# Performance work log

Hardware: AMD Instinct MI355X
Metric: run time of the kernel (lower is better)

## Reference

```python
import jax, jax.numpy as jnp
import numpy as np

N_NODES = 50000
N_EDGES = 1600000
D = 128


def setup_inputs() -> dict:
    key = jax.random.key(0)
    ks = jax.random.split(key, 12)
    feats = jax.random.normal(ks[0], (N_NODES, D), dtype=jnp.float32)
    src = jax.random.randint(ks[1], (N_EDGES,), 0, N_NODES)
    dst = jax.random.randint(ks[2], (N_EDGES,), 0, N_NODES)
    s = 1.0 / np.sqrt(D)
    inp = {"feats": feats, "src": src, "dst": dst}
    for i, k0 in enumerate(range(3, 12, 3)):
        inp[f"w_self{i}"] = jax.random.normal(ks[k0], (D, D), dtype=jnp.float32) * s
        inp[f"w_neigh{i}"] = jax.random.normal(ks[k0 + 1], (D, D), dtype=jnp.float32) * s
        inp[f"b{i}"] = jnp.zeros((D,), dtype=jnp.float32)
    return inp


def _sage_layer(h, src, dst, deg, w_self, w_neigh, b, act):
    # mean aggregation over incoming edges: gather src feats, scatter-sum to dst
    neigh_sum = jax.ops.segment_sum(h[src], dst, num_segments=N_NODES)  # [N, d]
    neigh = neigh_sum / deg[:, None]  # zero-degree nodes stay 0 (deg clamped to 1)
    out = h @ w_self + neigh @ w_neigh + b
    return jax.nn.relu(out) if act else out


def reference(feats, src, dst, w_self0, w_neigh0, b0, w_self1, w_neigh1, b1, w_self2, w_neigh2, b2):
    ones = jnp.ones((src.shape[0],), dtype=feats.dtype)
    deg = jax.ops.segment_sum(ones, dst, num_segments=N_NODES)
    deg = jnp.maximum(deg, 1.0)
    h = _sage_layer(feats, src, dst, deg, w_self0, w_neigh0, b0, True)
    h = _sage_layer(h, src, dst, deg, w_self1, w_neigh1, b1, True)
    h = _sage_layer(h, src, dst, deg, w_self2, w_neigh2, b2, False)
    return h
```

## Files before the change

### kernel.cpp

```cpp
#include <hip/hip_runtime.h>
#include <hip/hip_bf16.h>

#define N_NODES 50000
#define N_EDGES 1600000
#define DF 128
#define EPB 2500
#define B1 640
#define NBIN 196

typedef __attribute__((ext_vector_type(8))) short short8v;
typedef __attribute__((ext_vector_type(4))) float float4v;

__device__ __forceinline__ ushort bf16rne(float f) {
    uint u = __float_as_uint(f);
    return (ushort)((u + 0x7fffu + ((u >> 16) & 1u)) >> 16);
}


__global__ __launch_bounds__(256) void h1_kernel(const int* __restrict__ dst,
                                                 int* __restrict__ gh) {
    __shared__ int hist[NBIN];
    const int tid = threadIdx.x;
    const int blk = blockIdx.x;
    if (tid < NBIN) hist[tid] = 0;
    __syncthreads();
    const int lo = blk * EPB, hiE = min(lo + EPB, N_EDGES);
    for (int i = lo + tid; i < hiE; i += 256) atomicAdd(&hist[dst[i] >> 8], 1);
    __syncthreads();
    if (tid < NBIN) gh[tid * B1 + blk] = hist[tid];
}

__global__ __launch_bounds__(256) void scanA_kernel(int* __restrict__ gh,
                                                    int* __restrict__ rowtot) {
    __shared__ int buf[256];
    __shared__ int carry_s;
    const int tid = threadIdx.x;
    const int d = blockIdx.x;
    if (tid == 0) carry_s = 0;
    __syncthreads();
    for (int base = 0; base < B1; base += 256) {
        int idx = base + tid;
        int v = (idx < B1) ? gh[d * B1 + idx] : 0;
        buf[tid] = v;
        __syncthreads();
#pragma unroll
        for (int off = 1; off < 256; off <<= 1) {
            int t = (tid >= off) ? buf[tid - off] : 0;
            __syncthreads();
            buf[tid] += t;
            __syncthreads();
        }
        int carry = carry_s;
        if (idx < B1) gh[d * B1 + idx] = carry + buf[tid] - v;
        int tot = buf[255];
        __syncthreads();
        if (tid == 0) carry_s = carry + tot;
        __syncthreads();
    }
    if (tid == 0) rowtot[d] = carry_s;
}

__global__ __launch_bounds__(256) void scanB_kernel(const int* __restrict__ rowtot,
                                                    int* __restrict__ rowbase) {
    __shared__ int buf[256];
    const int tid = threadIdx.x;
    int v = (tid < NBIN) ? rowtot[tid] : 0;
    buf[tid] = v;
    __syncthreads();
#pragma unroll
    for (int off = 1; off < 256; off <<= 1) {
        int t = (tid >= off) ? buf[tid - off] : 0;
        __syncthreads();
        buf[tid] += t;
        __syncthreads();
    }
    if (tid < NBIN) rowbase[tid] = buf[tid] - v;
    if (tid == 0) rowbase[NBIN] = buf[255];
}

__global__ __launch_bounds__(256) void scatter1_kernel(const int* __restrict__ src,
                                                       const int* __restrict__ dst,
                                                       const int* __restrict__ gh,
                                                       const int* __restrict__ rowbase,
                                                       uint2* __restrict__ tmp) {
    __shared__ int cur[NBIN];
    const int tid = threadIdx.x;
    const int blk = blockIdx.x;
    if (tid < NBIN) cur[tid] = rowbase[tid] + gh[tid * B1 + blk];
    __syncthreads();
    const int lo = blk * EPB, hiE = min(lo + EPB, N_EDGES);
    for (int i = lo + tid; i < hiE; i += 256) {
        int d = dst[i];
        int pos = atomicAdd(&cur[d >> 8], 1);
        uint2 v;
        v.x = (uint)src[i];
        v.y = (uint)d;
        tmp[pos] = v;
    }
}

__global__ __launch_bounds__(256) void pass2_kernel(const uint2* __restrict__ tmp,
                                                    const int* __restrict__ rowbase,
                                                    int* __restrict__ deg,
                                                    int* __restrict__ rstart,
                                                    int* __restrict__ adj,
                                                    int* __restrict__ counter) {
    __shared__ int hist[256];
    __shared__ int sbuf[256];
    __shared__ int cur2[256];
    __shared__ int base_s;
    const int tid = threadIdx.x;
    const int hi = blockIdx.x;
    const int s = rowbase[hi], e = rowbase[hi + 1];
    hist[tid] = 0;
    __syncthreads();
    for (int i = s + tid; i < e; i += 256) atomicAdd(&hist[tmp[i].y & 255u], 1);
    __syncthreads();
    int h = hist[tid];
    int v = (h + 3) & ~3;
    sbuf[tid] = v;
    __syncthreads();
#pragma unroll
    for (int off = 1; off < 256; off <<= 1) {
        int t = (tid >= off) ? sbuf[tid - off] : 0;
        __syncthreads();
        sbuf[tid] += t;
        __syncthreads();
    }
    if (tid == 255) base_s = atomicAdd(counter, sbuf[255]);
    __syncthreads();
    int rs = base_s + sbuf[tid] - v;
    int n = hi * 256 + tid;
    if (n < N_NODES) {
        deg[n] = h;
        rstart[n] = rs;
    }
    cur2[tid] = rs;
    __syncthreads();
    for (int i = s + tid; i < e; i += 256) {
        uint2 t2 = tmp[i];
        int pos = atomicAdd(&cur2[t2.y & 255u], 1);
        adj[pos] = (int)t2.x;
    }
}


__global__ __launch_bounds__(256) void conv_kernel(const float* __restrict__ h,
                                                   ushort* __restrict__ hb) {
    int i = blockIdx.x * 256 + threadIdx.x;
    const int total = N_NODES * DF / 4;
    if (i < total) {
        float4 v = ((const float4*)h)[i];
        ushort4 o;
        o.x = bf16rne(v.x); o.y = bf16rne(v.y);
        o.z = bf16rne(v.z); o.w = bf16rne(v.w);
        ((ushort4*)hb)[i] = o;
    }
}


__global__ __launch_bounds__(256) void wprep_kernel(const float* __restrict__ wS,
                                                    const float* __restrict__ wN,
                                                    ushort* __restrict__ Wt) {
    int idx = blockIdx.x * 256 + threadIdx.x;
    if (idx < 128 * 256) {
        int c = idx >> 8;
        int k = idx & 255;
        float v = (k < 128) ? wS[k * 128 + c] : wN[(k - 128) * 128 + c];
        Wt[c * 256 + k] = bf16rne(v);
    }
}


__global__ __launch_bounds__(256) void agg_kernel(const ushort* __restrict__ hb,
                                                  const int* __restrict__ rstart,
                                                  const int* __restrict__ degv,
                                                  const int* __restrict__ adj,
                                                  ushort* __restrict__ neighb) {
    const int wave = threadIdx.x >> 6;
    const int lane = threadIdx.x & 63;
    const int n = blockIdx.x * 4 + wave;
    if (n >= N_NODES) return;
    const int s = rstart[n];
    const int d = degv[n];
    const int q = lane >> 4;
    const int f = lane & 15;
    const size_t foff = (size_t)(f * 8);

    float acc[8];
#pragma unroll
    for (int j = 0; j < 8; j++) acc[j] = 0.f;

#define GATHER_ADD(EIDX)                                                    \
    {                                                                       \
        int e_ = adj[(EIDX)];                                               \
        uint4 u_ = *(const uint4*)&hb[(size_t)e_ * DF + foff];              \
        acc[0] += __uint_as_float(u_.x << 16);                              \
        acc[1] += __uint_as_float(u_.x & 0xffff0000u);                      \
        acc[2] += __uint_as_float(u_.y << 16);                              \
        acc[3] += __uint_as_float(u_.y & 0xffff0000u);                      \
        acc[4] += __uint_as_float(u_.z << 16);                              \
        acc[5] += __uint_as_float(u_.z & 0xffff0000u);                      \
        acc[6] += __uint_as_float(u_.w << 16);                              \
        acc[7] += __uint_as_float(u_.w & 0xffff0000u);                      \
    }

    int i = 0;
    for (; i + 16 <= d; i += 16) {
        GATHER_ADD(s + i + q)
        GATHER_ADD(s + i + 4 + q)
        GATHER_ADD(s + i + 8 + q)
        GATHER_ADD(s + i + 12 + q)
    }
    for (; i + 4 <= d; i += 4) {
        GATHER_ADD(s + i + q)
    }
    if (i < d) {
        int r = d - i;
        if (q < r) GATHER_ADD(s + i + q)
    }
#undef GATHER_ADD

#pragma unroll
    for (int j = 0; j < 8; j++) {
        acc[j] += __shfl_xor(acc[j], 16, 64);
        acc[j] += __shfl_xor(acc[j], 32, 64);
    }

    if (q == 0) {
        float inv = 1.0f / (float)(d < 1 ? 1 : d);
        uint4 o;
        o.x = (uint)bf16rne(acc[0] * inv) | ((uint)bf16rne(acc[1] * inv) << 16);
        o.y = (uint)bf16rne(acc[2] * inv) | ((uint)bf16rne(acc[3] * inv) << 16);
        o.z = (uint)bf16rne(acc[4] * inv) | ((uint)bf16rne(acc[5] * inv) << 16);
        o.w = (uint)bf16rne(acc[6] * inv) | ((uint)bf16rne(acc[7] * inv) << 16);
        *(uint4*)&neighb[(size_t)n * DF + foff] = o;
    }
}


template <bool RELU, bool FP32OUT>
__global__ __launch_bounds__(256, 2) void gemm_mfma(const ushort* __restrict__ hbin,
                                                    const ushort* __restrict__ neighb,
                                                    const ushort* __restrict__ Wt,
                                                    const float* __restrict__ bias,
                                                    float* __restrict__ out32,
                                                    ushort* __restrict__ outbf) {
    __shared__ ushort As[64 * 40];
    __shared__ ushort Bs[128 * 40];
    const int tid = threadIdx.x;
    const int lane = tid & 63;
    const int w = tid >> 6;
    const int nbase = blockIdx.x * 64;
    const int l15 = lane & 15, l4 = lane >> 4;

    float4v acc[4][2];
#pragma unroll
    for (int i = 0; i < 4; i++)
#pragma unroll
        for (int j = 0; j < 2; j++) acc[i][j] = (float4v)0.f;

    for (int ks = 0; ks < 8; ++ks) {
        const int k0 = ks * 32;
        const ushort* Xsrc = (ks < 4) ? hbin : neighb;
        const int kk = k0 & 127;
        if (ks) __syncthreads();
        {
            int r = tid >> 2, cp = tid & 3;
            int gn = nbase + r;
            if (gn > N_NODES - 1) gn = N_NODES - 1;
            *(uint4*)&As[r * 40 + cp * 8] =
                *(const uint4*)&Xsrc[(size_t)gn * 128 + kk + cp * 8];
        }
#pragma unroll
        for (int j = 0; j < 2; j++) {
            int ch = tid + j * 256;
            int r = ch >> 2, cp = ch & 3;
            *(uint4*)&Bs[r * 40 + cp * 8] =
                *(const uint4*)&Wt[(size_t)r * 256 + k0 + cp * 8];
        }
        __syncthreads();
        short8v a[4], b[2];
#pragma unroll
        for (int i = 0; i < 4; i++)
            a[i] = *(const short8v*)&As[(i * 16 + l15) * 40 + l4 * 8];
#pragma unroll
        for (int j = 0; j < 2; j++)
            b[j] = *(const short8v*)&Bs[(w * 32 + j * 16 + l15) * 40 + l4 * 8];
#pragma unroll
        for (int i = 0; i < 4; i++)
#pragma unroll
            for (int j = 0; j < 2; j++)
                acc[i][j] = __builtin_amdgcn_mfma_f32_16x16x32_bf16(
                    a[i], b[j], acc[i][j], 0, 0, 0);
    }

#pragma unroll
    for (int j = 0; j < 2; j++) {
        int col = w * 32 + j * 16 + l15;
        float bv = bias[col];
#pragma unroll
        for (int i = 0; i < 4; i++) {
            int row0 = nbase + i * 16 + l4 * 4;
#pragma unroll
            for (int r = 0; r < 4; r++) {
                int row = row0 + r;
                if (row < N_NODES) {
                    float v = acc[i][j][r] + bv;
                    if (RELU) v = fmaxf(v, 0.f);
                    if (FP32OUT) {
                        out32[(size_t)row * 128 + col] = v;
                    } else {
                        outbf[(size_t)row * 128 + col] = bf16rne(v);
                    }
                }
            }
        }
    }
}


extern "C" void kernel_launch(void* const* d_in, const int* in_sizes, int n_in,
                              void* d_out, int out_size, void* d_ws, size_t ws_size,
                              hipStream_t stream) {
    const float* feats = (const float*)d_in[0];
    const int* src = (const int*)d_in[1];
    const int* dst = (const int*)d_in[2];
    const float* wS[3] = {(const float*)d_in[3], (const float*)d_in[6], (const float*)d_in[9]};
    const float* wN[3] = {(const float*)d_in[4], (const float*)d_in[7], (const float*)d_in[10]};
    const float* bb[3] = {(const float*)d_in[5], (const float*)d_in[8], (const float*)d_in[11]};
    float* out = (float*)d_out;

    char* p = (char*)d_ws;
    auto alloc = [&](size_t bytes) {
        char* r = p;
        p += (bytes + 255) & ~(size_t)255;
        return r;
    };
    ushort* hbA = (ushort*)alloc((size_t)N_NODES * DF * sizeof(ushort));
    ushort* hbB = (ushort*)alloc((size_t)N_NODES * DF * sizeof(ushort));
    ushort* neighb = (ushort*)alloc((size_t)N_NODES * DF * sizeof(ushort));
    ushort* Wt = (ushort*)alloc((size_t)3 * 128 * 256 * sizeof(ushort));
    uint2* tmp = (uint2*)alloc((size_t)N_EDGES * sizeof(uint2));
    int* gh = (int*)alloc((size_t)NBIN * B1 * sizeof(int));
    int* rowtot = (int*)alloc((size_t)NBIN * sizeof(int));
    int* rowbase = (int*)alloc((size_t)(NBIN + 1) * sizeof(int));
    int* deg = (int*)alloc((size_t)N_NODES * sizeof(int));
    int* rstart = (int*)alloc((size_t)N_NODES * sizeof(int));
    int* counter = (int*)alloc(sizeof(int));
    int* adj = (int*)alloc((size_t)(N_EDGES + 4 * N_NODES) * sizeof(int));

    const int CB = (N_NODES * DF / 4 + 255) / 256;
    const int WB = (128 * 256 + 255) / 256;

    hipMemsetAsync(counter, 0, sizeof(int), stream);
    h1_kernel<<<B1, 256, 0, stream>>>(dst, gh);
    scanA_kernel<<<NBIN, 256, 0, stream>>>(gh, rowtot);
    scanB_kernel<<<1, 256, 0, stream>>>(rowtot, rowbase);
    scatter1_kernel<<<B1, 256, 0, stream>>>(src, dst, gh, rowbase, tmp);
    pass2_kernel<<<NBIN, 256, 0, stream>>>(tmp, rowbase, deg, rstart, adj, counter);

    wprep_kernel<<<WB, 256, 0, stream>>>(wS[0], wN[0], Wt);
    wprep_kernel<<<WB, 256, 0, stream>>>(wS[1], wN[1], Wt + 128 * 256);
    wprep_kernel<<<WB, 256, 0, stream>>>(wS[2], wN[2], Wt + 2 * 128 * 256);
    conv_kernel<<<CB, 256, 0, stream>>>(feats, hbA);

    const int AGG_GRID = (N_NODES + 3) / 4;
    const int GB = (N_NODES + 63) / 64;

    agg_kernel<<<AGG_GRID, 256, 0, stream>>>(hbA, rstart, deg, adj, neighb);
    gemm_mfma<true, false><<<GB, 256, 0, stream>>>(hbA, neighb, Wt, bb[0], nullptr, hbB);
    agg_kernel<<<AGG_GRID, 256, 0, stream>>>(hbB, rstart, deg, adj, neighb);
    gemm_mfma<true, false><<<GB, 256, 0, stream>>>(hbB, neighb, Wt + 128 * 256, bb[1], nullptr, hbA);
    agg_kernel<<<AGG_GRID, 256, 0, stream>>>(hbA, rstart, deg, adj, neighb);
    gemm_mfma<false, true><<<GB, 256, 0, stream>>>(hbA, neighb, Wt + 2 * 128 * 256, bb[2], out, nullptr);
}
```

Baseline: 345.6 us.

## Fuse neighbor aggregation into GEMM layer kernel and merge prep kernels

Each layer's mean-aggregation is moved into the MFMA GEMM kernel. Each block gathers neighbor sums for its 64 rows into shared memory and uses them directly as the second half of the K dimension, which removes the neighb global round-trip and one launch per layer. The weight-transpose and feature-conversion kernels are merged into a single prep kernel, and the counter memset is folded into scanB. The trade-off is lower parallelism in the gather: 782 blocks each loop over 16 nodes per wave, instead of 12500 blocks with one node per wave. The larger shared-memory footprint may also cut occupancy and latency hiding for the random gathers.

```diff
diff --git a/kernel.cpp b/kernel.cpp
--- a/kernel.cpp
+++ b/kernel.cpp
@@ -61,7 +61,8 @@
 }
 
 __global__ __launch_bounds__(256) void scanB_kernel(const int* __restrict__ rowtot,
-                                                    int* __restrict__ rowbase) {
+                                                    int* __restrict__ rowbase,
+                                                    int* __restrict__ counter) {
     __shared__ int buf[256];
     const int tid = threadIdx.x;
     int v = (tid < NBIN) ? rowtot[tid] : 0;
@@ -75,7 +76,10 @@
         __syncthreads();
     }
     if (tid < NBIN) rowbase[tid] = buf[tid] - v;
-    if (tid == 0) rowbase[NBIN] = buf[255];
+    if (tid == 0) {
+        rowbase[NBIN] = buf[255];
+        counter[0] = 0;
+    }
 }
 
 __global__ __launch_bounds__(256) void scatter1_kernel(const int* __restrict__ src,
@@ -145,132 +149,133 @@
 }
 
 
-__global__ __launch_bounds__(256) void conv_kernel(const float* __restrict__ h,
-                                                   ushort* __restrict__ hb) {
-    int i = blockIdx.x * 256 + threadIdx.x;
-    const int total = N_NODES * DF / 4;
-    if (i < total) {
-        float4 v = ((const float4*)h)[i];
+#define CONV_TOT (N_NODES * DF / 4)
+#define WPREP_TOT (3 * 128 * 256)
+
+__global__ __launch_bounds__(256) void prep_kernel(const float* __restrict__ feats,
+                                                   ushort* __restrict__ hb,
+                                                   const float* __restrict__ wS0,
+                                                   const float* __restrict__ wN0,
+                                                   const float* __restrict__ wS1,
+                                                   const float* __restrict__ wN1,
+                                                   const float* __restrict__ wS2,
+                                                   const float* __restrict__ wN2,
+                                                   ushort* __restrict__ Wt) {
+    int gid = blockIdx.x * 256 + threadIdx.x;
+    if (gid < CONV_TOT) {
+        float4 v = ((const float4*)feats)[gid];
         ushort4 o;
         o.x = bf16rne(v.x); o.y = bf16rne(v.y);
         o.z = bf16rne(v.z); o.w = bf16rne(v.w);
-        ((ushort4*)hb)[i] = o;
-    }
-}
-
-
-__global__ __launch_bounds__(256) void wprep_kernel(const float* __restrict__ wS,
-                                                    const float* __restrict__ wN,
-                                                    ushort* __restrict__ Wt) {
-    int idx = blockIdx.x * 256 + threadIdx.x;
-    if (idx < 128 * 256) {
-        int c = idx >> 8;
-        int k = idx & 255;
-        float v = (k < 128) ? wS[k * 128 + c] : wN[(k - 128) * 128 + c];
-        Wt[c * 256 + k] = bf16rne(v);
-    }
-}
-
-
-__global__ __launch_bounds__(256) void agg_kernel(const ushort* __restrict__ hb,
-                                                  const int* __restrict__ rstart,
-                                                  const int* __restrict__ degv,
-                                                  const int* __restrict__ adj,
-                                                  ushort* __restrict__ neighb) {
-    const int wave = threadIdx.x >> 6;
-    const int lane = threadIdx.x & 63;
-    const int n = blockIdx.x * 4 + wave;
-    if (n >= N_NODES) return;
-    const int s = rstart[n];
-    const int d = degv[n];
-    const int q = lane >> 4;
-    const int f = lane & 15;
-    const size_t foff = (size_t)(f * 8);
-
-    float acc[8];
-#pragma unroll
-    for (int j = 0; j < 8; j++) acc[j] = 0.f;
-
-#define GATHER_ADD(EIDX)                                                    \
-    {                                                                       \
-        int e_ = adj[(EIDX)];                                               \
-        uint4 u_ = *(const uint4*)&hb[(size_t)e_ * DF + foff];              \
-        acc[0] += __uint_as_float(u_.x << 16);                              \
-        acc[1] += __uint_as_float(u_.x & 0xffff0000u);                      \
-        acc[2] += __uint_as_float(u_.y << 16);                              \
-        acc[3] += __uint_as_float(u_.y & 0xffff0000u);                      \
-        acc[4] += __uint_as_float(u_.z << 16);                              \
-        acc[5] += __uint_as_float(u_.z & 0xffff0000u);                      \
-        acc[6] += __uint_as_float(u_.w << 16);                              \
-        acc[7] += __uint_as_float(u_.w & 0xffff0000u);                      \
-    }
-
-    int i = 0;
-    for (; i + 16 <= d; i += 16) {
-        GATHER_ADD(s + i + q)
-        GATHER_ADD(s + i + 4 + q)
-        GATHER_ADD(s + i + 8 + q)
-        GATHER_ADD(s + i + 12 + q)
-    }
-    for (; i + 4 <= d; i += 4) {
-        GATHER_ADD(s + i + q)
-    }
-    if (i < d) {
-        int r = d - i;
-        if (q < r) GATHER_ADD(s + i + q)
-    }
-#undef GATHER_ADD
-
-#pragma unroll
-    for (int j = 0; j < 8; j++) {
-        acc[j] += __shfl_xor(acc[j], 16, 64);
-        acc[j] += __shfl_xor(acc[j], 32, 64);
-    }
-
-    if (q == 0) {
-        float inv = 1.0f / (float)(d < 1 ? 1 : d);
-        uint4 o;
-        o.x = (uint)bf16rne(acc[0] * inv) | ((uint)bf16rne(acc[1] * inv) << 16);
-        o.y = (uint)bf16rne(acc[2] * inv) | ((uint)bf16rne(acc[3] * inv) << 16);
-        o.z = (uint)bf16rne(acc[4] * inv) | ((uint)bf16rne(acc[5] * inv) << 16);
-        o.w = (uint)bf16rne(acc[6] * inv) | ((uint)bf16rne(acc[7] * inv) << 16);
-        *(uint4*)&neighb[(size_t)n * DF + foff] = o;
+        ((ushort4*)hb)[gid] = o;
+    } else {
+        int j = gid - CONV_TOT;
+        if (j < WPREP_TOT) {
+            int l = j >> 15;
+            int idx = j & 32767;
+            int c = idx >> 8;
+            int k = idx & 255;
+            const float* wS = (l == 0) ? wS0 : (l == 1) ? wS1 : wS2;
+            const float* wN = (l == 0) ? wN0 : (l == 1) ? wN1 : wN2;
+            float v = (k < 128) ? wS[k * 128 + c] : wN[(k - 128) * 128 + c];
+            Wt[(size_t)l * 128 * 256 + c * 256 + k] = bf16rne(v);
+        }
     }
 }
 
 
 template <bool RELU, bool FP32OUT>
-__global__ __launch_bounds__(256, 2) void gemm_mfma(const ushort* __restrict__ hbin,
-                                                    const ushort* __restrict__ neighb,
-                                                    const ushort* __restrict__ Wt,
-                                                    const float* __restrict__ bias,
-                                                    float* __restrict__ out32,
-                                                    ushort* __restrict__ outbf) {
+__global__ __launch_bounds__(256, 2) void layer_kernel(const ushort* __restrict__ hbin,
+                                                       const int* __restrict__ rstart,
+                                                       const int* __restrict__ degv,
+                                                       const int* __restrict__ adj,
+                                                       const ushort* __restrict__ Wt,
+                                                       const float* __restrict__ bias,
+                                                       float* __restrict__ out32,
+                                                       ushort* __restrict__ outbf) {
+    __shared__ ushort NT4[4 * 64 * 40];
     __shared__ ushort As[64 * 40];
     __shared__ ushort Bs[128 * 40];
     const int tid = threadIdx.x;
     const int lane = tid & 63;
     const int w = tid >> 6;
     const int nbase = blockIdx.x * 64;
+    const int q = lane >> 4;
+    const int f = lane & 15;
     const int l15 = lane & 15, l4 = lane >> 4;
 
-    float4v acc[4][2];
+    for (int t = 0; t < 16; ++t) {
+        const int ln = w * 16 + t;
+        const int n = nbase + ln;
+        float acc[8];
+#pragma unroll
+        for (int j = 0; j < 8; j++) acc[j] = 0.f;
+        int dd = 0;
+        if (n < N_NODES) {
+            const int s = rstart[n];
+            dd = degv[n];
+            const size_t foff = (size_t)(f * 8);
+#define GATHER_ADD(EIDX)                                                    \
+            {                                                               \
+                int e_ = adj[(EIDX)];                                       \
+                uint4 u_ = *(const uint4*)&hbin[(size_t)e_ * DF + foff];    \
+                acc[0] += __uint_as_float(u_.x << 16);                      \
+                acc[1] += __uint_as_float(u_.x & 0xffff0000u);              \
+                acc[2] += __uint_as_float(u_.y << 16);                      \
+                acc[3] += __uint_as_float(u_.y & 0xffff0000u);              \
+                acc[4] += __uint_as_float(u_.z << 16);                      \
+                acc[5] += __uint_as_float(u_.z & 0xffff0000u);              \
+                acc[6] += __uint_as_float(u_.w << 16);                      \
+                acc[7] += __uint_as_float(u_.w & 0xffff0000u);              \
+            }
+            int i = 0;
+            for (; i + 16 <= dd; i += 16) {
+                GATHER_ADD(s + i + q)
+                GATHER_ADD(s + i + 4 + q)
+                GATHER_ADD(s + i + 8 + q)
+                GATHER_ADD(s + i + 12 + q)
+            }
+            for (; i + 4 <= dd; i += 4) {
+                GATHER_ADD(s + i + q)
+            }
+            if (i < dd) {
+                int r = dd - i;
+                if (q < r) GATHER_ADD(s + i + q)
+            }
+#undef GATHER_ADD
+        }
+#pragma unroll
+        for (int j = 0; j < 8; j++) {
+            acc[j] += __shfl_xor(acc[j], 16, 64);
+            acc[j] += __shfl_xor(acc[j], 32, 64);
+        }
+        if (q == 0) {
+            float inv = 1.0f / (float)(dd < 1 ? 1 : dd);
+            uint4 o;
+            o.x = (uint)bf16rne(acc[0] * inv) | ((uint)bf16rne(acc[1] * inv) << 16);
+            o.y = (uint)bf16rne(acc[2] * inv) | ((uint)bf16rne(acc[3] * inv) << 16);
+            o.z = (uint)bf16rne(acc[4] * inv) | ((uint)bf16rne(acc[5] * inv) << 16);
+            o.w = (uint)bf16rne(acc[6] * inv) | ((uint)bf16rne(acc[7] * inv) << 16);
+            *(uint4*)&NT4[((f >> 2) * 64 + ln) * 40 + (f & 3) * 8] = o;
+        }
+    }
+    __syncthreads();
+
+    float4v gacc[4][2];
 #pragma unroll
     for (int i = 0; i < 4; i++)
 #pragma unroll
-        for (int j = 0; j < 2; j++) acc[i][j] = (float4v)0.f;
+        for (int j = 0; j < 2; j++) gacc[i][j] = (float4v)0.f;
 
     for (int ks = 0; ks < 8; ++ks) {
         const int k0 = ks * 32;
-        const ushort* Xsrc = (ks < 4) ? hbin : neighb;
-        const int kk = k0 & 127;
         if (ks) __syncthreads();
-        {
+        if (ks < 4) {
             int r = tid >> 2, cp = tid & 3;
             int gn = nbase + r;
             if (gn > N_NODES - 1) gn = N_NODES - 1;
             *(uint4*)&As[r * 40 + cp * 8] =
-                *(const uint4*)&Xsrc[(size_t)gn * 128 + kk + cp * 8];
+                *(const uint4*)&hbin[(size_t)gn * 128 + k0 + cp * 8];
         }
 #pragma unroll
         for (int j = 0; j < 2; j++) {
@@ -280,10 +285,11 @@
                 *(const uint4*)&Wt[(size_t)r * 256 + k0 + cp * 8];
         }
         __syncthreads();
+        const ushort* Atile = (ks < 4) ? As : &NT4[(ks - 4) * 64 * 40];
         short8v a[4], b[2];
 #pragma unroll
         for (int i = 0; i < 4; i++)
-            a[i] = *(const short8v*)&As[(i * 16 + l15) * 40 + l4 * 8];
+            a[i] = *(const short8v*)&Atile[(i * 16 + l15) * 40 + l4 * 8];
 #pragma unroll
         for (int j = 0; j < 2; j++)
             b[j] = *(const short8v*)&Bs[(w * 32 + j * 16 + l15) * 40 + l4 * 8];
@@ -291,8 +297,8 @@
         for (int i = 0; i < 4; i++)
 #pragma unroll
             for (int j = 0; j < 2; j++)
-                acc[i][j] = __builtin_amdgcn_mfma_f32_16x16x32_bf16(
-                    a[i], b[j], acc[i][j], 0, 0, 0);
+                gacc[i][j] = __builtin_amdgcn_mfma_f32_16x16x32_bf16(
+                    a[i], b[j], gacc[i][j], 0, 0, 0);
     }
 
 #pragma unroll
@@ -306,7 +312,7 @@
             for (int r = 0; r < 4; r++) {
                 int row = row0 + r;
                 if (row < N_NODES) {
-                    float v = acc[i][j][r] + bv;
+                    float v = gacc[i][j][r] + bv;
                     if (RELU) v = fmaxf(v, 0.f);
                     if (FP32OUT) {
                         out32[(size_t)row * 128 + col] = v;
@@ -339,7 +345,6 @@
     };
     ushort* hbA = (ushort*)alloc((size_t)N_NODES * DF * sizeof(ushort));
     ushort* hbB = (ushort*)alloc((size_t)N_NODES * DF * sizeof(ushort));
-    ushort* neighb = (ushort*)alloc((size_t)N_NODES * DF * sizeof(ushort));
     ushort* Wt = (ushort*)alloc((size_t)3 * 128 * 256 * sizeof(ushort));
     uint2* tmp = (uint2*)alloc((size_t)N_EDGES * sizeof(uint2));
     int* gh = (int*)alloc((size_t)NBIN * B1 * sizeof(int));
@@ -350,28 +355,22 @@
     int* counter = (int*)alloc(sizeof(int));
     int* adj = (int*)alloc((size_t)(N_EDGES + 4 * N_NODES) * sizeof(int));
 
-    const int CB = (N_NODES * DF / 4 + 255) / 256;
-    const int WB = (128 * 256 + 255) / 256;
-
-    hipMemsetAsync(counter, 0, sizeof(int), stream);
     h1_kernel<<<B1, 256, 0, stream>>>(dst, gh);
     scanA_kernel<<<NBIN, 256, 0, stream>>>(gh, rowtot);
-    scanB_kernel<<<1, 256, 0, stream>>>(rowtot, rowbase);
+    scanB_kernel<<<1, 256, 0, stream>>>(rowtot, rowbase, counter);
     scatter1_kernel<<<B1, 256, 0, stream>>>(src, dst, gh, rowbase, tmp);
     pass2_kernel<<<NBIN, 256, 0, stream>>>(tmp, rowbase, deg, rstart, adj, counter);
 
-    wprep_kernel<<<WB, 256, 0, stream>>>(wS[0], wN[0], Wt);
-    wprep_kernel<<<WB, 256, 0, stream>>>(wS[1], wN[1], Wt + 128 * 256);
-    wprep_kernel<<<WB, 256, 0, stream>>>(wS[2], wN[2], Wt + 2 * 128 * 256);
-    conv_kernel<<<CB, 256, 0, stream>>>(feats, hbA);
-
-    const int AGG_GRID = (N_NODES + 3) / 4;
+    const int PB = (CONV_TOT + WPREP_TOT + 255) / 256;
+    prep_kernel<<<PB, 256, 0, stream>>>(feats, hbA, wS[0], wN[0], wS[1], wN[1],
+                                        wS[2], wN[2], Wt);
+
     const int GB = (N_NODES + 63) / 64;
 
-    agg_kernel<<<AGG_GRID, 256, 0, stream>>>(hbA, rstart, deg, adj, neighb);
-    gemm_mfma<true, false><<<GB, 256, 0, stream>>>(hbA, neighb, Wt, bb[0], nullptr, hbB);
-    agg_kernel<<<AGG_GRID, 256, 0, stream>>>(hbB, rstart, deg, adj, neighb);
-    gemm_mfma<true, false><<<GB, 256, 0, stream>>>(hbB, neighb, Wt + 128 * 256, bb[1], nullptr, hbA);
-    agg_kernel<<<AGG_GRID, 256, 0, stream>>>(hbA, rstart, deg, adj, neighb);
-    gemm_mfma<false, true><<<GB, 256, 0, stream>>>(hbA, neighb, Wt + 2 * 128 * 256, bb[2], out, nullptr);
-}
+    layer_kernel<true, false><<<GB, 256, 0, stream>>>(hbA, rstart, deg, adj,
+                                                      Wt, bb[0], nullptr, hbB);
+    layer_kernel<true, false><<<GB, 256, 0, stream>>>(hbB, rstart, deg, adj,
+                                                      Wt + 128 * 256, bb[1], nullptr, hbA);
+    layer_kernel<false, true><<<GB, 256, 0, stream>>>(hbA, rstart, deg, adj,
+                                                      Wt + 2 * 128 * 256, bb[2], out, nullptr);
+}
```

Result: slower. 388.5 us (+12.4%).
